# Performance work log

Hardware: AMD Instinct MI355X
Metric: run time of the kernel (lower is better)

The kernel has to match this reference:

```python
import jax, jax.numpy as jnp
import numpy as np

NEIGHBOR_NUM = 4


def reference(vertices, feature_map, sample_idx):
    # vertices: (bs, n, 3), feature_map: (bs, n, c), sample_idx: (pool_num,)
    # pairwise squared distances: ||a||^2 + ||b||^2 - 2 a.b
    inner = jnp.einsum('bnd,bmd->bnm', vertices, vertices)  # (bs, n, n)
    quad = jnp.sum(vertices * vertices, axis=2)             # (bs, n)
    distance = -2.0 * inner + quad[:, None, :] + quad[:, :, None]
    # k+1 smallest distances (self is nearest); lax.top_k finds largest, so negate
    _, neighbor_index = jax.lax.top_k(-distance, NEIGHBOR_NUM + 1)
    neighbor_index = neighbor_index[:, :, 1:]               # drop self -> (bs, n, k)
    # gather neighbor features per batch: (bs, n, k, c)
    neighbor_feature = jax.vmap(lambda f, idx: f[idx])(feature_map, neighbor_index)
    pooled_feature = jnp.max(neighbor_feature, axis=2)      # (bs, n, c)
    vertices_pool = vertices[:, sample_idx, :]              # (bs, pool_num, 3)
    feature_map_pool = pooled_feature[:, sample_idx, :]     # (bs, pool_num, c)
    return vertices_pool, feature_map_pool


def setup_inputs() -> dict:
    key = jax.random.key(0)
    k1, k2 = jax.random.split(key)
    bs, n, c = 8, 4096, 256
    pool_num = n // 4
    vertices = jax.random.normal(k1, (bs, n, 3), dtype=jnp.float32)
    feature_map = jax.random.normal(k2, (bs, n, c), dtype=jnp.float32)
    sample_idx = jnp.arange(pool_num, dtype=jnp.int32)
    return {"vertices": vertices, "feature_map": feature_map, "sample_idx": sample_idx}
```

## Files before the change

### kernel.cpp

```cpp
#include <hip/hip_runtime.h>
#include <stdint.h>

#define BATCH 8
#define NPTS  4096
#define CH    256
#define QN    1024

#define SBLOCK 1024
#define SQPB   16
#define SBLOCKS_PER_BATCH (QN / SQPB)

__device__ __forceinline__ float fmul(float a, float b) { return __fmul_rn(a, b); }
__device__ __forceinline__ float fadd(float a, float b) { return __fadd_rn(a, b); }

__device__ __forceinline__ float cdist(const float4 vq, const float4 v) {
  float dot = fadd(fadd(fmul(vq.x, v.x), fmul(vq.y, v.y)), fmul(vq.z, v.z));
  return fadd(fadd(fmul(-2.0f, dot), v.w), vq.w);
}

__device__ __forceinline__ uint64_t mkkey(float d, uint32_t c) {
  uint32_t bb = __float_as_uint(d);
  bb ^= (uint32_t)((int32_t)bb >> 31) | 0x80000000u;
  return ((uint64_t)bb << 32) | c;
}

__device__ __forceinline__ void cswap(uint64_t& lo, uint64_t& hi) {
  uint64_t mn = hi < lo ? hi : lo;
  uint64_t mx = hi < lo ? lo : hi;
  lo = mn; hi = mx;
}

__device__ __forceinline__ uint64_t wave_min(uint64_t x) {
#define DPP_MIN_STEP(CTRL)                                                     \
  {                                                                            \
    uint32_t lo = (uint32_t)x, hi = (uint32_t)(x >> 32);                       \
    uint32_t rl = (uint32_t)__builtin_amdgcn_update_dpp((int)lo, (int)lo,      \
                                                        CTRL, 0xF, 0xF, false);\
    uint32_t rh = (uint32_t)__builtin_amdgcn_update_dpp((int)hi, (int)hi,      \
                                                        CTRL, 0xF, 0xF, false);\
    uint64_t o = ((uint64_t)rh << 32) | rl;                                    \
    x = o < x ? o : x;                                                         \
  }
  DPP_MIN_STEP(0x121)
  DPP_MIN_STEP(0x122)
  DPP_MIN_STEP(0x124)
  DPP_MIN_STEP(0x128)
#undef DPP_MIN_STEP
  { uint64_t o = (uint64_t)__shfl_xor((long long)x, 16, 64); x = o < x ? o : x; }
  { uint64_t o = (uint64_t)__shfl_xor((long long)x, 32, 64); x = o < x ? o : x; }
  return x;
}

__shared__ float4 sv[NPTS];

__global__ __launch_bounds__(SBLOCK) void knn_scan_kernel(
    const float* __restrict__ verts,
    const int*   __restrict__ sidx,
    int4*        __restrict__ nbr,
    float*       __restrict__ outV)
{
  const int batch = blockIdx.x / SBLOCKS_PER_BATCH;
  const int qblk  = blockIdx.x % SBLOCKS_PER_BATCH;
  const float* vb = verts + (size_t)batch * (NPTS * 3);

  for (int c = threadIdx.x; c < NPTS; c += SBLOCK) {
    float x = vb[c * 3 + 0];
    float y = vb[c * 3 + 1];
    float z = vb[c * 3 + 2];
    float q = fadd(fadd(fmul(x, x), fmul(y, y)), fmul(z, z));
    sv[c] = make_float4(x, y, z, q);
  }
  __syncthreads();

  const int wave = threadIdx.x >> 6;
  const int lane = threadIdx.x & 63;
  const int i = qblk * SQPB + wave;
  const float4 vq = sv[sidx[i]];

  float    d0 = __builtin_inff(), d1 = __builtin_inff();
  uint32_t i0 = 0, i1 = 0;
#pragma unroll 16
  for (int t = 0; t < NPTS / 64; ++t) {
    float4 v = sv[lane + t * 64];
    const uint32_t c = lane + t * 64;
    float d = cdist(vq, v);
    bool lt = d < d1;
    d1 = lt ? d : d1;
    i1 = lt ? c : i1;
    bool sw = d1 < d0;
    float    td = d0;  uint32_t ti = i0;
    d0 = sw ? d1 : d0;  i0 = sw ? i1 : i0;
    d1 = sw ? td : d1;  i1 = sw ? ti : i1;
  }

  uint64_t k0 = mkkey(d0, i0);
  uint64_t k1 = mkkey(d1, i1);
  uint64_t prev = 0, nb1 = 0, nb2 = 0, nb3 = 0, nb4 = 0;
#pragma unroll
  for (int r = 0; r < 5; ++r) {
    uint64_t cand = k0 > prev ? k0 : (k1 > prev ? k1 : ~0ull);
    cand = wave_min(cand);
    if (r == 1) nb1 = cand;
    if (r == 2) nb2 = cand;
    if (r == 3) nb3 = cand;
    if (r == 4) nb4 = cand;
    prev = cand;
  }
  if (__any(k1 < nb4)) {
    uint64_t b0 = ~0ull, b1 = ~0ull, b2 = ~0ull, b3 = ~0ull, b4 = ~0ull;
    for (int t = 0; t < NPTS / 64; ++t) {
      float4 v = sv[lane + t * 64];
      uint64_t key = mkkey(cdist(vq, v), lane + t * 64);
      b4 = key < b4 ? key : b4;
      cswap(b3, b4); cswap(b2, b3); cswap(b1, b2); cswap(b0, b1);
    }
    prev = 0;
#pragma unroll
    for (int r = 0; r < 5; ++r) {
      uint64_t cand = b0 > prev ? b0
                    : b1 > prev ? b1
                    : b2 > prev ? b2
                    : b3 > prev ? b3
                    : b4 > prev ? b4 : ~0ull;
      cand = wave_min(cand);
      if (r == 1) nb1 = cand;
      if (r == 2) nb2 = cand;
      if (r == 3) nb3 = cand;
      if (r == 4) nb4 = cand;
      prev = cand;
    }
  }

  if (lane == 0) {
    nbr[(size_t)batch * QN + i] = make_int4((int)(uint32_t)nb1,
                                            (int)(uint32_t)nb2,
                                            (int)(uint32_t)nb3,
                                            (int)(uint32_t)nb4);
  }
  if (lane < 3) {
    float val = lane == 0 ? vq.x : (lane == 1 ? vq.y : vq.z);
    outV[((size_t)batch * QN + i) * 3 + lane] = val;
  }
}

#define GBLOCK 256
#define GQPB   (GBLOCK / 64)

__global__ __launch_bounds__(GBLOCK) void knn_gather_kernel(
    const float* __restrict__ feat,
    const int4*  __restrict__ nbr,
    float*       __restrict__ outF)
{
  const int gq   = blockIdx.x * GQPB + (threadIdx.x >> 6);
  const int lane = threadIdx.x & 63;
  const int4 nb  = nbr[gq];
  const int batch = gq >> 10;
  const float* fb = feat + (size_t)batch * NPTS * CH;
  const int col = lane * 4;

  float4 f1 = *(const float4*)(fb + (size_t)nb.x * CH + col);
  float4 f2 = *(const float4*)(fb + (size_t)nb.y * CH + col);
  float4 f3 = *(const float4*)(fb + (size_t)nb.z * CH + col);
  float4 f4 = *(const float4*)(fb + (size_t)nb.w * CH + col);
  float4 r;
  r.x = fmaxf(fmaxf(f1.x, f2.x), fmaxf(f3.x, f4.x));
  r.y = fmaxf(fmaxf(f1.y, f2.y), fmaxf(f3.y, f4.y));
  r.z = fmaxf(fmaxf(f1.z, f2.z), fmaxf(f3.z, f4.z));
  r.w = fmaxf(fmaxf(f1.w, f2.w), fmaxf(f3.w, f4.w));
  *(float4*)(outF + (size_t)gq * CH + col) = r;
}

extern "C" void kernel_launch(void* const* d_in, const int* in_sizes, int n_in,
                              void* d_out, int out_size, void* d_ws, size_t ws_size,
                              hipStream_t stream) {
  const float* verts = (const float*)d_in[0];
  const float* feat  = (const float*)d_in[1];
  const int*   sidx  = (const int*)d_in[2];
  float* outV = (float*)d_out;
  float* outF = (float*)d_out + (size_t)BATCH * QN * 3;
  int4*  nbr  = (int4*)d_ws;

  knn_scan_kernel<<<dim3(BATCH * SBLOCKS_PER_BATCH), dim3(SBLOCK), 0, stream>>>(
      verts, sidx, nbr, outV);
  knn_gather_kernel<<<dim3(BATCH * QN / GQPB), dim3(GBLOCK), 0, stream>>>(
      feat, nbr, outF);
}
```

Measured before the change: 45.03 us.

## Precompute padded vertex+norm array in a prep kernel and scan from global memory

A new prep kernel writes each vertex as a float4 (x,y,z,|v|^2) to workspace once. The scan kernel then reads candidates straight from global memory (through L1/L2) instead of staging all 4096 points per block in LDS. This drops the per-block staging loop, its barrier and the 64 KB of shared memory, which should allow more resident blocks. The unroll factor drops and the launch bounds gain a min-blocks hint. The trade-off is an extra kernel launch and inner-loop loads served by cache rather than LDS.

```diff
diff --git a/kernel.cpp b/kernel.cpp
--- a/kernel.cpp
+++ b/kernel.cpp
@@ -5,10 +5,6 @@
 #define NPTS  4096
 #define CH    256
 #define QN    1024
-
-#define SBLOCK 1024
-#define SQPB   16
-#define SBLOCKS_PER_BATCH (QN / SQPB)
 
 __device__ __forceinline__ float fmul(float a, float b) { return __fmul_rn(a, b); }
 __device__ __forceinline__ float fadd(float a, float b) { return __fadd_rn(a, b); }
@@ -51,37 +47,42 @@
   return x;
 }
 
-__shared__ float4 sv[NPTS];
+__global__ __launch_bounds__(256) void prep_kernel(
+    const float* __restrict__ verts,
+    float4*      __restrict__ vc)
+{
+  const int p = blockIdx.x * 256 + threadIdx.x;
+  const float x = verts[p * 3 + 0];
+  const float y = verts[p * 3 + 1];
+  const float z = verts[p * 3 + 2];
+  const float q = fadd(fadd(fmul(x, x), fmul(y, y)), fmul(z, z));
+  vc[p] = make_float4(x, y, z, q);
+}
 
-__global__ __launch_bounds__(SBLOCK) void knn_scan_kernel(
-    const float* __restrict__ verts,
-    const int*   __restrict__ sidx,
-    int4*        __restrict__ nbr,
-    float*       __restrict__ outV)
+#define SBLOCK 1024
+#define SQPB   16
+#define SBLOCKS_PER_BATCH (QN / SQPB)
+
+__global__ __launch_bounds__(SBLOCK, 8) void knn_scan_kernel(
+    const float4* __restrict__ vc,
+    const int*    __restrict__ sidx,
+    int4*         __restrict__ nbr,
+    float*        __restrict__ outV)
 {
   const int batch = blockIdx.x / SBLOCKS_PER_BATCH;
   const int qblk  = blockIdx.x % SBLOCKS_PER_BATCH;
-  const float* vb = verts + (size_t)batch * (NPTS * 3);
-
-  for (int c = threadIdx.x; c < NPTS; c += SBLOCK) {
-    float x = vb[c * 3 + 0];
-    float y = vb[c * 3 + 1];
-    float z = vb[c * 3 + 2];
-    float q = fadd(fadd(fmul(x, x), fmul(y, y)), fmul(z, z));
-    sv[c] = make_float4(x, y, z, q);
-  }
-  __syncthreads();
+  const float4* vb = vc + (size_t)batch * NPTS;
 
   const int wave = threadIdx.x >> 6;
   const int lane = threadIdx.x & 63;
   const int i = qblk * SQPB + wave;
-  const float4 vq = sv[sidx[i]];
+  const float4 vq = vb[sidx[i]];
 
   float    d0 = __builtin_inff(), d1 = __builtin_inff();
   uint32_t i0 = 0, i1 = 0;
-#pragma unroll 16
+#pragma unroll 8
   for (int t = 0; t < NPTS / 64; ++t) {
-    float4 v = sv[lane + t * 64];
+    float4 v = vb[lane + t * 64];
     const uint32_t c = lane + t * 64;
     float d = cdist(vq, v);
     bool lt = d < d1;
@@ -109,7 +110,7 @@
   if (__any(k1 < nb4)) {
     uint64_t b0 = ~0ull, b1 = ~0ull, b2 = ~0ull, b3 = ~0ull, b4 = ~0ull;
     for (int t = 0; t < NPTS / 64; ++t) {
-      float4 v = sv[lane + t * 64];
+      float4 v = vb[lane + t * 64];
       uint64_t key = mkkey(cdist(vq, v), lane + t * 64);
       b4 = key < b4 ? key : b4;
       cswap(b3, b4); cswap(b2, b3); cswap(b1, b2); cswap(b0, b1);
@@ -178,10 +179,13 @@
   const int*   sidx  = (const int*)d_in[2];
   float* outV = (float*)d_out;
   float* outF = (float*)d_out + (size_t)BATCH * QN * 3;
-  int4*  nbr  = (int4*)d_ws;
 
+  float4* vc  = (float4*)d_ws;
+  int4*   nbr = (int4*)((char*)d_ws + (size_t)BATCH * NPTS * sizeof(float4));
+
+  prep_kernel<<<dim3(BATCH * NPTS / 256), dim3(256), 0, stream>>>(verts, vc);
   knn_scan_kernel<<<dim3(BATCH * SBLOCKS_PER_BATCH), dim3(SBLOCK), 0, stream>>>(
-      verts, sidx, nbr, outV);
+      vc, sidx, nbr, outV);
   knn_gather_kernel<<<dim3(BATCH * QN / GQPB), dim3(GBLOCK), 0, stream>>>(
       feat, nbr, outF);
 }
```

After: 54.08 us. +20.1%, slower.
